# Kernel tuning notes

Hardware: AMD Instinct MI355X
Metric: run time of the kernel (lower is better)

## Reference

```python
import jax, jax.numpy as jnp
import numpy as np

B, S, N, D = 8, 2048, 4096, 256
MAX_W = 16  # fixed cap on span width (torch code derives it from data; padding is masked)
TINY = 1e-13  # allennlp util.masked_mean clamp


def setup_inputs() -> dict:
    key = jax.random.key(0)
    k1, k2, k3 = jax.random.split(key, 3)
    sequence_tensor = jax.random.normal(k1, (B, S, D), dtype=jnp.float32)
    starts = jax.random.randint(k2, (B, N, 1), 0, S - MAX_W)
    widths = jax.random.randint(k3, (B, N, 1), 0, MAX_W)  # width in [0, MAX_W-1]
    span_indices = jnp.concatenate([starts, starts + widths], axis=-1)  # [B,N,2], ends >= starts
    return {"sequence_tensor": sequence_tensor, "span_indices": span_indices}


def reference(sequence_tensor, span_indices):
    starts = span_indices[..., 0:1]            # [B,N,1]
    ends = span_indices[..., 1:2]              # [B,N,1]
    widths = ends - starts                     # [B,N,1]
    rng = jnp.arange(MAX_W)[None, None, :]     # [1,1,W]
    raw_idx = ends - rng                       # [B,N,W] indices counting back from end
    span_mask = ((rng <= widths) & (raw_idx >= 0)).astype(sequence_tensor.dtype)  # [B,N,W]
    idx = jnp.maximum(raw_idx, 0)              # relu(raw).long()
    batch_ids = jnp.arange(sequence_tensor.shape[0])[:, None, None]
    span_embeddings = sequence_tensor[batch_ids, idx]  # gather -> [B,N,W,D]
    summed = jnp.einsum('bnwd,bnw->bnd', span_embeddings, span_mask)
    count = jnp.maximum(jnp.sum(span_mask, axis=-1, keepdims=True), TINY)  # [B,N,1]
    return summed / count  # masked mean over span positions -> [B,N,D]
```

## Files before the change

kernel.cpp:

```cpp
#include <hip/hip_runtime.h>

#define PB 8
#define PS 2048
#define PN 4096
#define PD 256

typedef float f4 __attribute__((ext_vector_type(4)));

__global__ __launch_bounds__(256, 8) void span_mean_kernel(
    const float* __restrict__ seq,
    const int*   __restrict__ spans,
    float*       __restrict__ out)
{
    const int b       = blockIdx.x & 7;
    const int blk     = blockIdx.x >> 3;
    const int span_ib = (blk << 2) | (threadIdx.x >> 6);
    const int span    = (b << 12) | span_ib;
    const int lane    = threadIdx.x & 63;

    const int2 se    = ((const int2*)spans)[span];
    const int  start = __builtin_amdgcn_readfirstlane(se.x);
    const int  width = __builtin_amdgcn_readfirstlane(se.y - se.x);

    const float inv = 1.0f / (float)(width + 1);

    const f4* b4 = (const f4*)(seq + (((size_t)b * PS + (size_t)start) * PD)) + lane;

    f4 v[8];
#pragma unroll
    for (int r = 0; r < 8; ++r) v[r] = b4[r * 64];

    f4 acc = v[0];
#pragma unroll
    for (int r = 1; r < 8; ++r) {
        const float m = (width >= r) ? 1.0f : 0.0f;
        acc += v[r] * m;
    }

    if (width >= 8) {
        f4 u[8];
#pragma unroll
        for (int r = 0; r < 8; ++r) u[r] = b4[(8 + r) * 64];

        acc += u[0];
#pragma unroll
        for (int r = 1; r < 8; ++r) {
            const float m = (width >= 8 + r) ? 1.0f : 0.0f;
            acc += u[r] * m;
        }
    }

    acc *= inv;

    f4* outp = (f4*)(out + (size_t)span * PD) + lane;
    __builtin_nontemporal_store(acc, outp);
}

extern "C" void kernel_launch(void* const* d_in, const int* in_sizes, int n_in,
                              void* d_out, int out_size, void* d_ws, size_t ws_size,
                              hipStream_t stream) {
    const float* seq   = (const float*)d_in[0];
    const int*   spans = (const int*)d_in[1];
    float*       out   = (float*)d_out;

    const int n_spans = PB * PN;
    dim3 grid(n_spans / 4);
    dim3 block(256);
    span_mean_kernel<<<grid, block, 0, stream>>>(seq, spans, out);
}
```

Before: 88.83 us.

## Replace per-span gather sums with chunked prefix sums over the sequence

Adds a first kernel that computes running sums inside chunks of 32 positions and records per-chunk totals in workspace. The span kernel then builds each span sum from at most three vector loads (end prefix, start-1 prefix, and a chunk total when the span crosses a chunk boundary), instead of loading up to 16 rows. This removes most of the gather traffic and arithmetic. In exchange it costs an extra pass that reads and writes the full sequence, a second launch, and small float cancellation error from subtracting prefixes.

```diff
diff --git a/kernel.cpp b/kernel.cpp
--- a/kernel.cpp
+++ b/kernel.cpp
@@ -4,11 +4,36 @@
 #define PS 2048
 #define PN 4096
 #define PD 256
+#define CHUNK 32
+#define NCH (PS / CHUNK)
 
 typedef float f4 __attribute__((ext_vector_type(4)));
 
-__global__ __launch_bounds__(256, 8) void span_mean_kernel(
+__global__ __launch_bounds__(256) void chunk_prefix_kernel(
     const float* __restrict__ seq,
+    float*       __restrict__ P,
+    float*       __restrict__ T)
+{
+    const int b = blockIdx.x & 7;
+    const int c = blockIdx.x >> 3;
+    const int d = threadIdx.x;
+
+    const size_t base = ((size_t)b * PS + (size_t)c * CHUNK) * PD + (size_t)d;
+    const float* sp = seq + base;
+    float*       pp = P   + base;
+
+    float run = 0.0f;
+#pragma unroll
+    for (int s = 0; s < CHUNK; ++s) {
+        run += __builtin_nontemporal_load(sp + (size_t)s * PD);
+        pp[(size_t)s * PD] = run;
+    }
+    T[((size_t)b * NCH + c) * PD + (size_t)d] = run;
+}
+
+__global__ __launch_bounds__(256) void span_mean_kernel(
+    const float* __restrict__ P,
+    const float* __restrict__ T,
     const int*   __restrict__ spans,
     float*       __restrict__ out)
 {
@@ -20,36 +45,23 @@
 
     const int2 se    = ((const int2*)spans)[span];
     const int  start = __builtin_amdgcn_readfirstlane(se.x);
-    const int  width = __builtin_amdgcn_readfirstlane(se.y - se.x);
+    const int  end   = __builtin_amdgcn_readfirstlane(se.y);
+    const int  width = end - start;
 
     const float inv = 1.0f / (float)(width + 1);
 
-    const f4* b4 = (const f4*)(seq + (((size_t)b * PS + (size_t)start) * PD)) + lane;
+    const int   sm = (start > 0) ? (start - 1) : 0;
+    const float m0 = (start > 0) ? 1.0f : 0.0f;
+    const int   cs = sm >> 5;
+    const int   ce = end >> 5;
+    const float mt = (ce > cs) ? 1.0f : 0.0f;
 
-    f4 v[8];
-#pragma unroll
-    for (int r = 0; r < 8; ++r) v[r] = b4[r * 64];
+    const f4* Pb = (const f4*)(P + (size_t)b * PS * PD) + lane;
+    const f4 pe = Pb[(size_t)end * 64];
+    const f4 ps = Pb[(size_t)sm  * 64];
+    const f4 tt = ((const f4*)(T + ((size_t)b * NCH + (size_t)cs) * PD))[lane];
 
-    f4 acc = v[0];
-#pragma unroll
-    for (int r = 1; r < 8; ++r) {
-        const float m = (width >= r) ? 1.0f : 0.0f;
-        acc += v[r] * m;
-    }
-
-    if (width >= 8) {
-        f4 u[8];
-#pragma unroll
-        for (int r = 0; r < 8; ++r) u[r] = b4[(8 + r) * 64];
-
-        acc += u[0];
-#pragma unroll
-        for (int r = 1; r < 8; ++r) {
-            const float m = (width >= 8 + r) ? 1.0f : 0.0f;
-            acc += u[r] * m;
-        }
-    }
-
+    f4 acc = pe - ps * m0 + tt * mt;
     acc *= inv;
 
     f4* outp = (f4*)(out + (size_t)span * PD) + lane;
@@ -63,8 +75,11 @@
     const int*   spans = (const int*)d_in[1];
     float*       out   = (float*)d_out;
 
+    float* P = (float*)d_ws;
+    float* T = P + (size_t)PB * PS * PD;
+
+    chunk_prefix_kernel<<<dim3(PB * NCH), dim3(256), 0, stream>>>(seq, P, T);
+
     const int n_spans = PB * PN;
-    dim3 grid(n_spans / 4);
-    dim3 block(256);
-    span_mean_kernel<<<grid, block, 0, stream>>>(seq, spans, out);
+    span_mean_kernel<<<dim3(n_spans / 4), dim3(256), 0, stream>>>(P, T, spans, out);
 }
```

Result: no change. 87.09 us (-2.0%).
